# Kernel tuning notes

Hardware: AMD Instinct MI355X
Metric: run time of the kernel (lower is better)

The kernel has to match this reference:

```python
import jax, jax.numpy as jnp
import numpy as np

N = 1048576

def _init_linear(key, fan_in, fan_out):
    # torch nn.Linear default init: U(-1/sqrt(fan_in), 1/sqrt(fan_in))
    kw, kb = jax.random.split(key)
    bound = 1.0 / np.sqrt(fan_in)
    W = jax.random.uniform(kw, (fan_out, fan_in), jnp.float32, -bound, bound)
    b = jax.random.uniform(kb, (fan_out,), jnp.float32, -bound, bound)
    return W, b

def setup_inputs() -> dict:
    key = jax.random.key(0)
    kx, k1, k2, k3, k4 = jax.random.split(key, 5)
    x = jax.random.normal(kx, (N, 6), dtype=jnp.float32)
    W1, b1 = _init_linear(k1, 6, 128)
    W2, b2 = _init_linear(k2, 128, 128)
    W3, b3 = _init_linear(k3, 128, 128)
    W4, b4 = _init_linear(k4, 128, 4)
    return {"x": x, "W1": W1, "b1": b1, "W2": W2, "b2": b2,
            "W3": W3, "b3": b3, "W4": W4, "b4": b4}

def reference(x, W1, b1, W2, b2, W3, b3, W4, b4):
    h = jax.nn.relu(x @ W1.T + b1)          # [N,128]
    h = jax.nn.relu(h @ W2.T + b2)          # [N,128]
    h = jax.nn.relu(h @ W3.T + b3)          # [N,128]
    return h @ W4.T + b4                     # [N,4]
```

## Files before the change

kernel.cpp:

```cpp
#include <hip/hip_runtime.h>


typedef __attribute__((ext_vector_type(8))) short short8;
typedef __attribute__((ext_vector_type(4))) float f32x4;
typedef __attribute__((ext_vector_type(2))) float f32x2;
typedef __attribute__((ext_vector_type(4))) unsigned int u32x4;

#define MFMA(a, b, c) __builtin_amdgcn_mfma_f32_16x16x32_bf16((a), (b), (c), 0, 0, 0)

__device__ __forceinline__ unsigned short bfr(float f) {
  unsigned u = __builtin_bit_cast(unsigned, f);
  u += 0x7FFFu + ((u >> 16) & 1u);
  return (unsigned short)(u >> 16);
}

__device__ __forceinline__ unsigned pk2(float a, float b) {
  unsigned r;
  asm("v_cvt_pk_bf16_f32 %0, %1, %2" : "=v"(r) : "v"(a), "v"(b));
  return r;
}

__device__ __forceinline__ unsigned pkrelu(float a, float b) {
  a = __builtin_fmaxf(a, 0.f);
  b = __builtin_fmaxf(b, 0.f);
  return pk2(a, b);
}

__device__ __forceinline__ short8 pack4(const f32x4& a0, const f32x4& a1) {
  u32x4 u;
  u.x = pkrelu(a0.x, a0.y);
  u.y = pkrelu(a0.z, a0.w);
  u.z = pkrelu(a1.x, a1.y);
  u.w = pkrelu(a1.z, a1.w);
  return __builtin_bit_cast(short8, u);
}

__device__ __forceinline__ int sig_inv(int kp) {
  return ((kp >> 5) << 5) + (((kp >> 2) & 1) << 4) + (((kp >> 3) & 3) << 2) + (kp & 3);
}

__global__ void nerf_stage(const float* __restrict__ W1, const float* __restrict__ b1,
                           const float* __restrict__ W2, const float* __restrict__ b2,
                           const float* __restrict__ W3, const float* __restrict__ b3,
                           const float* __restrict__ W4, const float* __restrict__ b4,
                           void* __restrict__ ws) {
  unsigned short* wf = (unsigned short*)ws;
  const int idx = blockIdx.x * 256 + threadIdx.x;
  const int stride = gridDim.x * 256;

  for (int p = idx; p < 64 * 64; p += stride) {
    const int f = p >> 6, l = p & 63, m = l & 15, q = l >> 4;
    const int g = f & 31, ks = g >> 3, nt = g & 7;
    const float* W = (f < 32) ? W2 : W3;
    unsigned short v[8];
#pragma unroll
    for (int j = 0; j < 8; ++j)
      v[j] = bfr(W[(nt * 16 + m) * 128 + sig_inv(ks * 32 + q * 8 + j)]);
#pragma unroll
    for (int j = 0; j < 8; ++j) wf[f * 512 + l * 8 + j] = v[j];
  }

  for (int e = idx; e < 128; e += stride) {
    const int nt = e >> 4, n = e & 15;
    unsigned short v[8];
#pragma unroll
    for (int j = 0; j < 8; ++j) {
      float val = 0.f;
      if (j < 6) val = W1[(nt * 16 + n) * 6 + j];
      else if (j == 6) val = b1[nt * 16 + n];
      v[j] = bfr(val);
    }
#pragma unroll
    for (int j = 0; j < 8; ++j) wf[(65536 >> 1) + e * 8 + j] = v[j];
  }

  for (int e = idx; e < 64; e += stride) {
    const int ks = e >> 4, s = e & 15, q = s >> 2, n = s & 3;
    unsigned short v[8];
#pragma unroll
    for (int j = 0; j < 8; ++j)
      v[j] = bfr(W4[n * 128 + sig_inv(ks * 32 + q * 8 + j)]);
#pragma unroll
    for (int j = 0; j < 8; ++j) wf[(67584 >> 1) + e * 8 + j] = v[j];
  }

  {
    float* z = (float*)((char*)ws + 68608);
    for (int e = idx; e < 512; e += stride) z[e] = 0.f;
  }

  {
    float* wb = (float*)((char*)ws + 70656);
    for (int e = idx; e < 272; e += stride) {
      float val;
      if (e < 128) val = b2[e];
      else if (e < 256) val = b3[e - 128];
      else val = ((e & 15) < 4) ? b4[e & 3] : 0.f;
      wb[e] = val;
    }
  }
}

__launch_bounds__(1024, 4)
__global__ void nerf_main(const float* __restrict__ x, float* __restrict__ out,
                          const void* __restrict__ ws, int nGroups) {
  __shared__ __align__(16) unsigned short lds[32768];

  {
    const u32x4* src = (const u32x4*)ws;
    u32x4* dst = (u32x4*)lds;
    for (int i = threadIdx.x; i < 4096; i += 1024) dst[i] = src[i];
  }
  __syncthreads();

  const int lane = threadIdx.x & 63;
  const int wid = threadIdx.x >> 6;
  const int q = lane >> 4;
  const int n = lane & 15;

  {
    const int ws4 = wid & 3;
    if (ws4 == 1) __builtin_amdgcn_s_sleep(8);
    else if (ws4 == 2) __builtin_amdgcn_s_sleep(16);
    else if (ws4 == 3) __builtin_amdgcn_s_sleep(24);
  }

  const int waveId = blockIdx.x * 16 + wid;
  const int totalWaves = gridDim.x * 16;

  const unsigned short* w2b = lds + lane * 8;
  const unsigned short* w3b = lds + 16384 + lane * 8;

  const int l1off = ((q == 0) ? 65536 : 68608) + n * 16;
  const int l4off = (n < 4) ? (67584 + (q * 4 + n) * 16) : (68608 + n * 16);
  const int b2off = 70656 + q * 16;
  const int b3off = 71168 + q * 16;
  const int b4off = 71680 + q * 16;

  const f32x4 zf = {0.f, 0.f, 0.f, 0.f};

  float px[2][6] = {};
  int g = waveId;
  if (g < nGroups && q == 0) {
#pragma unroll
    for (int t = 0; t < 2; ++t) {
      const float* p = x + (g * 32 + t * 16 + n) * 6;
      f32x2 a = *(const f32x2*)p, b = *(const f32x2*)(p + 2), c = *(const f32x2*)(p + 4);
      px[t][0] = a.x; px[t][1] = a.y; px[t][2] = b.x;
      px[t][3] = b.y; px[t][4] = c.x; px[t][5] = c.y;
    }
  }

  for (; g < nGroups; g += totalWaves) {
    uintptr_t wsl = (uintptr_t)ws;
    asm volatile("" : "+v"(wsl));
    const char* wsv = (const char*)wsl;
    const short8* l1g = (const short8*)(wsv + l1off);
    const short8* l4g = (const short8*)(wsv + l4off);
    const f32x4* bias2 = (const f32x4*)(wsv + b2off);
    const f32x4* bias3 = (const f32x4*)(wsv + b3off);
    const f32x4* b4p   = (const f32x4*)(wsv + b4off);

    short8 xb[2];
#pragma unroll
    for (int t = 0; t < 2; ++t) {
      u32x4 u = {0u, 0u, 0u, 0u};
      if (q == 0) {
        u.x = pk2(px[t][0], px[t][1]);
        u.y = pk2(px[t][2], px[t][3]);
        u.z = pk2(px[t][4], px[t][5]);
        u.w = 0x00003F80u;
      }
      xb[t] = __builtin_bit_cast(short8, u);
    }
    const int gn = g + totalWaves;
    if (gn < nGroups && q == 0) {
#pragma unroll
      for (int t = 0; t < 2; ++t) {
        const float* p = x + (gn * 32 + t * 16 + n) * 6;
        f32x2 a = *(const f32x2*)p, b = *(const f32x2*)(p + 2), c = *(const f32x2*)(p + 4);
        px[t][0] = a.x; px[t][1] = a.y; px[t][2] = b.x;
        px[t][3] = b.y; px[t][4] = c.x; px[t][5] = c.y;
      }
    }

    short8 B1[2][4], B2[2][4];

#pragma unroll
    for (int ntp = 0; ntp < 4; ++ntp) {
      const short8 w0 = l1g[(2 * ntp) * 16];
      const short8 w1 = l1g[(2 * ntp + 1) * 16];
      f32x4 a0[2], a1[2];
#pragma unroll
      for (int t = 0; t < 2; ++t) {
        a0[t] = MFMA(w0, xb[t], zf);
        a1[t] = MFMA(w1, xb[t], zf);
      }
#pragma unroll
      for (int t = 0; t < 2; ++t) B1[t][ntp] = pack4(a0[t], a1[t]);
    }

#pragma unroll
    for (int ntp = 0; ntp < 4; ++ntp) {
      f32x4 a0[2], a1[2];
#pragma unroll
      for (int ks = 0; ks < 4; ++ks) {
        const short8 w0 = *(const short8*)(w2b + (ks * 8 + 2 * ntp) * 512);
        const short8 w1 = *(const short8*)(w2b + (ks * 8 + 2 * ntp + 1) * 512);
        if (ks == 0) {
          const f32x4 bv0 = bias2[(2 * ntp) * 4];
          const f32x4 bv1 = bias2[(2 * ntp + 1) * 4];
#pragma unroll
          for (int t = 0; t < 2; ++t) {
            a0[t] = MFMA(w0, B1[t][0], bv0);
            a1[t] = MFMA(w1, B1[t][0], bv1);
          }
        } else {
#pragma unroll
          for (int t = 0; t < 2; ++t) {
            a0[t] = MFMA(w0, B1[t][ks], a0[t]);
            a1[t] = MFMA(w1, B1[t][ks], a1[t]);
          }
        }
      }
#pragma unroll
      for (int t = 0; t < 2; ++t) B2[t][ntp] = pack4(a0[t], a1[t]);
    }

#pragma unroll
    for (int ntp = 0; ntp < 4; ++ntp) {
      f32x4 a0[2], a1[2];
#pragma unroll
      for (int ks = 0; ks < 4; ++ks) {
        const short8 w0 = *(const short8*)(w3b + (ks * 8 + 2 * ntp) * 512);
        const short8 w1 = *(const short8*)(w3b + (ks * 8 + 2 * ntp + 1) * 512);
        if (ks == 0) {
          const f32x4 bv0 = bias3[(2 * ntp) * 4];
          const f32x4 bv1 = bias3[(2 * ntp + 1) * 4];
#pragma unroll
          for (int t = 0; t < 2; ++t) {
            a0[t] = MFMA(w0, B2[t][0], bv0);
            a1[t] = MFMA(w1, B2[t][0], bv1);
          }
        } else {
#pragma unroll
          for (int t = 0; t < 2; ++t) {
            a0[t] = MFMA(w0, B2[t][ks], a0[t]);
            a1[t] = MFMA(w1, B2[t][ks], a1[t]);
          }
        }
      }
#pragma unroll
      for (int t = 0; t < 2; ++t) B1[t][ntp] = pack4(a0[t], a1[t]);
    }

    f32x4 o[2];
    {
      const f32x4 bv = b4p[0];
#pragma unroll
      for (int ks = 0; ks < 4; ++ks) {
        const short8 w = l4g[ks * 16];
        if (ks == 0) {
#pragma unroll
          for (int t = 0; t < 2; ++t) o[t] = MFMA(w, B1[t][0], bv);
        } else {
#pragma unroll
          for (int t = 0; t < 2; ++t) o[t] = MFMA(w, B1[t][ks], o[t]);
        }
      }
    }
    if (q == 0) {
#pragma unroll
      for (int t = 0; t < 2; ++t)
        *(f32x4*)(out + (g * 32 + t * 16 + n) * 4) = o[t];
    }
  }
}

extern "C" void kernel_launch(void* const* d_in, const int* in_sizes, int n_in,
                              void* d_out, int out_size, void* d_ws, size_t ws_size,
                              hipStream_t stream) {
  const float* x  = (const float*)d_in[0];
  const float* W1 = (const float*)d_in[1];
  const float* b1 = (const float*)d_in[2];
  const float* W2 = (const float*)d_in[3];
  const float* b2 = (const float*)d_in[4];
  const float* W3 = (const float*)d_in[5];
  const float* b3 = (const float*)d_in[6];
  const float* W4 = (const float*)d_in[7];
  const float* b4 = (const float*)d_in[8];
  float* out = (float*)d_out;

  const int N = in_sizes[0] / 6;
  const int nGroups = N / 32;

  nerf_stage<<<dim3(4), dim3(256), 0, stream>>>(W1, b1, W2, b2, W3, b3, W4, b4, d_ws);

  nerf_main<<<dim3(512), dim3(1024), 0, stream>>>(x, out, d_ws, nGroups);
}
```

Measured before the change: 158.2 us.

## Switch MLP layers from 16x16x32 to 32x32x16 bf16 MFMA tiles

Replaces the 16x16x32 bf16 MFMA path with 32x32x16 MFMA, processing 32 points per wave as a single tile instead of two 16-point tiles. Weight fragments are re-laid out for the 32x32 operand format with a new k-permutation. Layer-1 bias is now folded into the accumulator init instead of a constant-one input column. The larger tile halves the number of LDS weight fragment reads per point and reduces MFMA instruction count. The cost is larger accumulators (16 floats each) and possible changes in register pressure or latency per instruction.

```diff
diff --git a/kernel.cpp b/kernel.cpp
--- a/kernel.cpp
+++ b/kernel.cpp
@@ -3,10 +3,11 @@
 
 typedef __attribute__((ext_vector_type(8))) short short8;
 typedef __attribute__((ext_vector_type(4))) float f32x4;
+typedef __attribute__((ext_vector_type(16))) float f32x16;
 typedef __attribute__((ext_vector_type(2))) float f32x2;
 typedef __attribute__((ext_vector_type(4))) unsigned int u32x4;
 
-#define MFMA(a, b, c) __builtin_amdgcn_mfma_f32_16x16x32_bf16((a), (b), (c), 0, 0, 0)
+#define MFMA32(a, b, c) __builtin_amdgcn_mfma_f32_32x32x16_bf16((a), (b), (c), 0, 0, 0)
 
 __device__ __forceinline__ unsigned short bfr(float f) {
   unsigned u = __builtin_bit_cast(unsigned, f);
@@ -26,17 +27,36 @@
   return pk2(a, b);
 }
 
-__device__ __forceinline__ short8 pack4(const f32x4& a0, const f32x4& a1) {
+__device__ __forceinline__ short8 pack8lo(const f32x16& c) {
   u32x4 u;
-  u.x = pkrelu(a0.x, a0.y);
-  u.y = pkrelu(a0.z, a0.w);
-  u.z = pkrelu(a1.x, a1.y);
-  u.w = pkrelu(a1.z, a1.w);
+  u.x = pkrelu(c[0], c[1]);
+  u.y = pkrelu(c[2], c[3]);
+  u.z = pkrelu(c[4], c[5]);
+  u.w = pkrelu(c[6], c[7]);
   return __builtin_bit_cast(short8, u);
 }
 
-__device__ __forceinline__ int sig_inv(int kp) {
-  return ((kp >> 5) << 5) + (((kp >> 2) & 1) << 4) + (((kp >> 3) & 3) << 2) + (kp & 3);
+__device__ __forceinline__ short8 pack8hi(const f32x16& c) {
+  u32x4 u;
+  u.x = pkrelu(c[8], c[9]);
+  u.y = pkrelu(c[10], c[11]);
+  u.z = pkrelu(c[12], c[13]);
+  u.w = pkrelu(c[14], c[15]);
+  return __builtin_bit_cast(short8, u);
+}
+
+__device__ __forceinline__ f32x16 ldbias(const char* p) {
+  const f32x4 b0 = *(const f32x4*)(p);
+  const f32x4 b1 = *(const f32x4*)(p + 32);
+  const f32x4 b2 = *(const f32x4*)(p + 64);
+  const f32x4 b3 = *(const f32x4*)(p + 96);
+  f32x16 a = {b0.x, b0.y, b0.z, b0.w, b1.x, b1.y, b1.z, b1.w,
+              b2.x, b2.y, b2.z, b2.w, b3.x, b3.y, b3.z, b3.w};
+  return a;
+}
+
+__device__ __forceinline__ int sig32(int kp) {
+  return (kp & ~12) | ((kp & 4) << 1) | ((kp & 8) >> 1);
 }
 
 __global__ void nerf_stage(const float* __restrict__ W1, const float* __restrict__ b1,
@@ -49,55 +69,52 @@
   const int stride = gridDim.x * 256;
 
   for (int p = idx; p < 64 * 64; p += stride) {
-    const int f = p >> 6, l = p & 63, m = l & 15, q = l >> 4;
-    const int g = f & 31, ks = g >> 3, nt = g & 7;
+    const int f = p >> 6, l = p & 63, m = l & 31, hi = l >> 5;
+    const int g = f & 31, i = g >> 3, ks = g & 7;
     const float* W = (f < 32) ? W2 : W3;
     unsigned short v[8];
 #pragma unroll
     for (int j = 0; j < 8; ++j)
-      v[j] = bfr(W[(nt * 16 + m) * 128 + sig_inv(ks * 32 + q * 8 + j)]);
+      v[j] = bfr(W[(i * 32 + m) * 128 + sig32(ks * 16 + hi * 8 + j)]);
 #pragma unroll
     for (int j = 0; j < 8; ++j) wf[f * 512 + l * 8 + j] = v[j];
   }
 
   for (int e = idx; e < 128; e += stride) {
-    const int nt = e >> 4, n = e & 15;
+    const int i = e >> 5, m = e & 31;
     unsigned short v[8];
 #pragma unroll
-    for (int j = 0; j < 8; ++j) {
-      float val = 0.f;
-      if (j < 6) val = W1[(nt * 16 + n) * 6 + j];
-      else if (j == 6) val = b1[nt * 16 + n];
-      v[j] = bfr(val);
-    }
-#pragma unroll
-    for (int j = 0; j < 8; ++j) wf[(65536 >> 1) + e * 8 + j] = v[j];
+    for (int j = 0; j < 8; ++j)
+      v[j] = (j < 6) ? bfr(W1[(i * 32 + m) * 6 + j]) : (unsigned short)0;
+#pragma unroll
+    for (int j = 0; j < 8; ++j) wf[32768 + i * 256 + m * 8 + j] = v[j];
   }
 
   for (int e = idx; e < 64; e += stride) {
-    const int ks = e >> 4, s = e & 15, q = s >> 2, n = s & 3;
+    const int ks = e >> 3, s = e & 7, hi = s >> 2, m = s & 3;
     unsigned short v[8];
 #pragma unroll
     for (int j = 0; j < 8; ++j)
-      v[j] = bfr(W4[n * 128 + sig_inv(ks * 32 + q * 8 + j)]);
-#pragma unroll
-    for (int j = 0; j < 8; ++j) wf[(67584 >> 1) + e * 8 + j] = v[j];
-  }
-
-  {
-    float* z = (float*)((char*)ws + 68608);
+      v[j] = bfr(W4[m * 128 + sig32(ks * 16 + hi * 8 + j)]);
+#pragma unroll
+    for (int j = 0; j < 8; ++j) wf[33792 + ks * 64 + s * 8 + j] = v[j];
+  }
+
+  {
+    float* fb = (float*)((char*)ws + 68608);
+    for (int e = idx; e < 416; e += stride) {
+      float val;
+      if (e < 128) val = b1[e];
+      else if (e < 256) val = b2[e - 128];
+      else if (e < 384) val = b3[e - 256];
+      else val = ((e - 384) < 4) ? b4[e - 384] : 0.f;
+      fb[e] = val;
+    }
+  }
+
+  {
+    float* z = (float*)((char*)ws + 70272);
     for (int e = idx; e < 512; e += stride) z[e] = 0.f;
-  }
-
-  {
-    float* wb = (float*)((char*)ws + 70656);
-    for (int e = idx; e < 272; e += stride) {
-      float val;
-      if (e < 128) val = b2[e];
-      else if (e < 256) val = b3[e - 128];
-      else val = ((e & 15) < 4) ? b4[e & 3] : 0.f;
-      wb[e] = val;
-    }
   }
 }
 
@@ -115,8 +132,8 @@
 
   const int lane = threadIdx.x & 63;
   const int wid = threadIdx.x >> 6;
-  const int q = lane >> 4;
-  const int n = lane & 15;
+  const int hi = lane >> 5;
+  const int m = lane & 31;
 
   {
     const int ws4 = wid & 3;
@@ -128,151 +145,86 @@
   const int waveId = blockIdx.x * 16 + wid;
   const int totalWaves = gridDim.x * 16;
 
-  const unsigned short* w2b = lds + lane * 8;
-  const unsigned short* w3b = lds + 16384 + lane * 8;
-
-  const int l1off = ((q == 0) ? 65536 : 68608) + n * 16;
-  const int l4off = (n < 4) ? (67584 + (q * 4 + n) * 16) : (68608 + n * 16);
-  const int b2off = 70656 + q * 16;
-  const int b3off = 71168 + q * 16;
-  const int b4off = 71680 + q * 16;
-
-  const f32x4 zf = {0.f, 0.f, 0.f, 0.f};
-
-  float px[2][6] = {};
+  const unsigned short* w2l = lds + lane * 8;
+  const unsigned short* w3l = lds + 16384 + lane * 8;
+
+  const int l1off = ((hi == 0) ? 0 : 4736) + m * 16;
+  const int l4off = (m < 4) ? (2048 + (hi * 4 + m) * 16) : (4736 + m * 16);
+  const int bOff = 3072 + hi * 16;
+
+  float px[6];
   int g = waveId;
-  if (g < nGroups && q == 0) {
-#pragma unroll
-    for (int t = 0; t < 2; ++t) {
-      const float* p = x + (g * 32 + t * 16 + n) * 6;
-      f32x2 a = *(const f32x2*)p, b = *(const f32x2*)(p + 2), c = *(const f32x2*)(p + 4);
-      px[t][0] = a.x; px[t][1] = a.y; px[t][2] = b.x;
-      px[t][3] = b.y; px[t][4] = c.x; px[t][5] = c.y;
-    }
+  if (g < nGroups && hi == 0) {
+    const float* p = x + (g * 32 + m) * 6;
+    f32x2 a = *(const f32x2*)p, b = *(const f32x2*)(p + 2), c = *(const f32x2*)(p + 4);
+    px[0] = a.x; px[1] = a.y; px[2] = b.x; px[3] = b.y; px[4] = c.x; px[5] = c.y;
   }
 
   for (; g < nGroups; g += totalWaves) {
     uintptr_t wsl = (uintptr_t)ws;
     asm volatile("" : "+v"(wsl));
-    const char* wsv = (const char*)wsl;
-    const short8* l1g = (const short8*)(wsv + l1off);
-    const short8* l4g = (const short8*)(wsv + l4off);
-    const f32x4* bias2 = (const f32x4*)(wsv + b2off);
-    const f32x4* bias3 = (const f32x4*)(wsv + b3off);
-    const f32x4* b4p   = (const f32x4*)(wsv + b4off);
-
-    short8 xb[2];
-#pragma unroll
-    for (int t = 0; t < 2; ++t) {
+    const char* eA = (const char*)wsl + 65536;
+    const char* l1p = eA + l1off;
+    const char* l4p = eA + l4off;
+    const char* bp = eA + bOff;
+
+    short8 xb;
+    {
       u32x4 u = {0u, 0u, 0u, 0u};
-      if (q == 0) {
-        u.x = pk2(px[t][0], px[t][1]);
-        u.y = pk2(px[t][2], px[t][3]);
-        u.z = pk2(px[t][4], px[t][5]);
-        u.w = 0x00003F80u;
+      if (hi == 0) {
+        u.x = pk2(px[0], px[1]);
+        u.y = pk2(px[2], px[3]);
+        u.z = pk2(px[4], px[5]);
       }
-      xb[t] = __builtin_bit_cast(short8, u);
+      xb = __builtin_bit_cast(short8, u);
     }
     const int gn = g + totalWaves;
-    if (gn < nGroups && q == 0) {
-#pragma unroll
-      for (int t = 0; t < 2; ++t) {
-        const float* p = x + (gn * 32 + t * 16 + n) * 6;
-        f32x2 a = *(const f32x2*)p, b = *(const f32x2*)(p + 2), c = *(const f32x2*)(p + 4);
-        px[t][0] = a.x; px[t][1] = a.y; px[t][2] = b.x;
-        px[t][3] = b.y; px[t][4] = c.x; px[t][5] = c.y;
+    if (gn < nGroups && hi == 0) {
+      const float* p = x + (gn * 32 + m) * 6;
+      f32x2 a = *(const f32x2*)p, b = *(const f32x2*)(p + 2), c = *(const f32x2*)(p + 4);
+      px[0] = a.x; px[1] = a.y; px[2] = b.x; px[3] = b.y; px[4] = c.x; px[5] = c.y;
+    }
+
+    short8 B1f[8], B2f[8];
+
+#pragma unroll
+    for (int i = 0; i < 4; ++i) {
+      const short8 w = *(const short8*)(l1p + i * 512);
+      f32x16 acc = ldbias(bp + i * 128);
+      acc = MFMA32(w, xb, acc);
+      B1f[2 * i] = pack8lo(acc);
+      B1f[2 * i + 1] = pack8hi(acc);
+    }
+
+#pragma unroll
+    for (int i = 0; i < 4; ++i) {
+      f32x16 acc = ldbias(bp + 512 + i * 128);
+#pragma unroll
+      for (int ks = 0; ks < 8; ++ks)
+        acc = MFMA32(*(const short8*)(w2l + (i * 8 + ks) * 512), B1f[ks], acc);
+      B2f[2 * i] = pack8lo(acc);
+      B2f[2 * i + 1] = pack8hi(acc);
+    }
+
+#pragma unroll
+    for (int i = 0; i < 4; ++i) {
+      f32x16 acc = ldbias(bp + 1024 + i * 128);
+#pragma unroll
+      for (int ks = 0; ks < 8; ++ks)
+        acc = MFMA32(*(const short8*)(w3l + (i * 8 + ks) * 512), B2f[ks], acc);
+      B1f[2 * i] = pack8lo(acc);
+      B1f[2 * i + 1] = pack8hi(acc);
+    }
+
+    {
+      f32x16 acc = ldbias(bp + 1536);
+#pragma unroll
+      for (int ks = 0; ks < 8; ++ks)
+        acc = MFMA32(*(const short8*)(l4p + ks * 128), B1f[ks], acc);
+      if (hi == 0) {
+        f32x4 o = {acc[0], acc[1], acc[2], acc[3]};
+        *(f32x4*)(out + (g * 32 + m) * 4) = o;
       }
-    }
-
-    short8 B1[2][4], B2[2][4];
-
-#pragma unroll
-    for (int ntp = 0; ntp < 4; ++ntp) {
-      const short8 w0 = l1g[(2 * ntp) * 16];
-      const short8 w1 = l1g[(2 * ntp + 1) * 16];
-      f32x4 a0[2], a1[2];
-#pragma unroll
-      for (int t = 0; t < 2; ++t) {
-        a0[t] = MFMA(w0, xb[t], zf);
-        a1[t] = MFMA(w1, xb[t], zf);
-      }
-#pragma unroll
-      for (int t = 0; t < 2; ++t) B1[t][ntp] = pack4(a0[t], a1[t]);
-    }
-
-#pragma unroll
-    for (int ntp = 0; ntp < 4; ++ntp) {
-      f32x4 a0[2], a1[2];
-#pragma unroll
-      for (int ks = 0; ks < 4; ++ks) {
-        const short8 w0 = *(const short8*)(w2b + (ks * 8 + 2 * ntp) * 512);
-        const short8 w1 = *(const short8*)(w2b + (ks * 8 + 2 * ntp + 1) * 512);
-        if (ks == 0) {
-          const f32x4 bv0 = bias2[(2 * ntp) * 4];
-          const f32x4 bv1 = bias2[(2 * ntp + 1) * 4];
-#pragma unroll
-          for (int t = 0; t < 2; ++t) {
-            a0[t] = MFMA(w0, B1[t][0], bv0);
-            a1[t] = MFMA(w1, B1[t][0], bv1);
-          }
-        } else {
-#pragma unroll
-          for (int t = 0; t < 2; ++t) {
-            a0[t] = MFMA(w0, B1[t][ks], a0[t]);
-            a1[t] = MFMA(w1, B1[t][ks], a1[t]);
-          }
-        }
-      }
-#pragma unroll
-      for (int t = 0; t < 2; ++t) B2[t][ntp] = pack4(a0[t], a1[t]);
-    }
-
-#pragma unroll
-    for (int ntp = 0; ntp < 4; ++ntp) {
-      f32x4 a0[2], a1[2];
-#pragma unroll
-      for (int ks = 0; ks < 4; ++ks) {
-        const short8 w0 = *(const short8*)(w3b + (ks * 8 + 2 * ntp) * 512);
-        const short8 w1 = *(const short8*)(w3b + (ks * 8 + 2 * ntp + 1) * 512);
-        if (ks == 0) {
-          const f32x4 bv0 = bias3[(2 * ntp) * 4];
-          const f32x4 bv1 = bias3[(2 * ntp + 1) * 4];
-#pragma unroll
-          for (int t = 0; t < 2; ++t) {
-            a0[t] = MFMA(w0, B2[t][0], bv0);
-            a1[t] = MFMA(w1, B2[t][0], bv1);
-          }
-        } else {
-#pragma unroll
-          for (int t = 0; t < 2; ++t) {
-            a0[t] = MFMA(w0, B2[t][ks], a0[t]);
-            a1[t] = MFMA(w1, B2[t][ks], a1[t]);
-          }
-        }
-      }
-#pragma unroll
-      for (int t = 0; t < 2; ++t) B1[t][ntp] = pack4(a0[t], a1[t]);
-    }
-
-    f32x4 o[2];
-    {
-      const f32x4 bv = b4p[0];
-#pragma unroll
-      for (int ks = 0; ks < 4; ++ks) {
-        const short8 w = l4g[ks * 16];
-        if (ks == 0) {
-#pragma unroll
-          for (int t = 0; t < 2; ++t) o[t] = MFMA(w, B1[t][0], bv);
-        } else {
-#pragma unroll
-          for (int t = 0; t < 2; ++t) o[t] = MFMA(w, B1[t][ks], o[t]);
-        }
-      }
-    }
-    if (q == 0) {
-#pragma unroll
-      for (int t = 0; t < 2; ++t)
-        *(f32x4*)(out + (g * 32 + t * 16 + n) * 4) = o[t];
     }
   }
 }
```

Result: slower. 168.1 us (+6.2%).
